# Optimization experiments

Hardware: AMD Instinct MI355X
Metric: run time of the kernel (lower is better)

The kernel has to match this reference:

```python
import jax, jax.numpy as jnp
import numpy as np

B, N = 2, 512
CS, CZ = 512, 128
H, C, PQ, PV = 8, 16, 8, 12
INF, EPS = 1e5, 1e-8


def _points(s, W, b, P):
    # OpenFold layout: [*, N, 3*H*P] split into 3 chunks (x, y, z), stacked on last dim
    p = (s @ W + b).reshape(s.shape[0], s.shape[1], 3, H, P)
    return jnp.moveaxis(p, 2, -1)  # [b, n, H, P, 3]


def setup_inputs() -> dict:
    key = jax.random.key(0)
    ks = jax.random.split(key, 10)
    sc = 0.02
    cat_dim = H * C + H * PV * 4 + H * CZ  # o, o_pt(x,y,z), o_pt_norm, o_pair
    return {
        "seqs": jax.random.normal(ks[0], (B, N, CS), jnp.float32),
        "pair_rep": jax.random.normal(ks[1], (B, N, N, CZ), jnp.float32) * 0.1,
        "x_t": jax.random.normal(ks[2], (B, N, 3), jnp.float32) * 10.0,
        "mask": jnp.ones((B, N), jnp.float32),
        "Wq": jax.random.normal(ks[3], (CS, H * C), jnp.float32) * sc,
        "bq": jnp.zeros((H * C,), jnp.float32),
        "Wkv": jax.random.normal(ks[4], (CS, H * 2 * C), jnp.float32) * sc,
        "bkv": jnp.zeros((H * 2 * C,), jnp.float32),
        "Wqp": jax.random.normal(ks[5], (CS, H * PQ * 3), jnp.float32) * sc,
        "bqp": jnp.zeros((H * PQ * 3,), jnp.float32),
        "Wkvp": jax.random.normal(ks[6], (CS, H * (PQ + PV) * 3), jnp.float32) * sc,
        "bkvp": jnp.zeros((H * (PQ + PV) * 3,), jnp.float32),
        "Wb": jax.random.normal(ks[7], (CZ, H), jnp.float32) * sc,
        "bb": jnp.zeros((H,), jnp.float32),
        "head_w": jnp.zeros((H,), jnp.float32),
        "Wout": jax.random.normal(ks[8], (cat_dim, CS), jnp.float32) * sc,
        "bout": jnp.zeros((CS,), jnp.float32),
    }


def reference(seqs, pair_rep, x_t, mask, Wq, bq, Wkv, bkv, Wqp, bqp, Wkvp, bkvp,
              Wb, bb, head_w, Wout, bout):
    b, n = seqs.shape[0], seqs.shape[1]
    t = x_t * mask[..., None]  # masked translations; rotations are identity

    # scalar q, k, v
    q = (seqs @ Wq + bq).reshape(b, n, H, C)
    kv = (seqs @ Wkv + bkv).reshape(b, n, H, 2 * C)
    k, v = kv[..., :C], kv[..., C:]

    # point q, k, v in global frame (identity rotation => just translate)
    q_pts = _points(seqs, Wqp, bqp, PQ) + t[:, :, None, None, :]      # [b,n,H,PQ,3]
    kv_pts = _points(seqs, Wkvp, bkvp, PQ + PV) + t[:, :, None, None, :]
    k_pts, v_pts = kv_pts[:, :, :, :PQ], kv_pts[:, :, :, PQ:]          # [b,n,H,PQ|PV,3]

    # pair bias
    bias = pair_rep @ Wb + bb                                          # [b,n,n,H]

    # scalar attention logits
    w_l = np.sqrt(1.0 / (3 * C)).astype(np.float32)
    a = jnp.einsum('bihc,bjhc->bhij', q, k) * w_l
    a = a + np.sqrt(1.0 / 3).astype(np.float32) * jnp.transpose(bias, (0, 3, 1, 2))

    # point attention: sum_p |q_ihp - k_jhp|^2 = |q|^2 + |k|^2 - 2 q.k (summed over p,xyz)
    sq_q = jnp.transpose(jnp.sum(q_pts ** 2, axis=(-1, -2)), (0, 2, 1))  # [b,H,n]
    sq_k = jnp.transpose(jnp.sum(k_pts ** 2, axis=(-1, -2)), (0, 2, 1))
    cross = jnp.einsum('bihpx,bjhpx->bhij', q_pts, k_pts)
    d2 = sq_q[..., :, None] + sq_k[..., None, :] - 2.0 * cross           # [b,H,i,j]
    w_c = np.sqrt(1.0 / (3 * (PQ * 9.0 / 2))).astype(np.float32)
    hw = jax.nn.softplus(head_w) * w_c                                   # [H]
    a = a - 0.5 * hw[None, :, None, None] * d2

    # mask
    sq_mask = INF * (mask[:, :, None] * mask[:, None, :] - 1.0)          # [b,n,n]
    a = jax.nn.softmax(a + sq_mask[:, None], axis=-1)                    # [b,H,i,j]

    # outputs
    o = jnp.einsum('bhij,bjhc->bihc', a, v).reshape(b, n, H * C)
    o_pt = jnp.einsum('bhij,bjhpx->bihpx', a, v_pts)                     # [b,n,H,PV,3]
    o_pt = o_pt - t[:, :, None, None, :]                                 # invert_apply (identity rot)
    o_pt_norm = jnp.sqrt(jnp.sum(o_pt ** 2, axis=-1) + EPS).reshape(b, n, H * PV)
    o_pt_flat = o_pt.reshape(b, n, H * PV, 3)
    o_pt_xyz = jnp.concatenate([o_pt_flat[..., 0], o_pt_flat[..., 1], o_pt_flat[..., 2]], axis=-1)
    o_pair = jnp.einsum('bhij,bijz->bihz', a, pair_rep).reshape(b, n, H * CZ)

    feats = jnp.concatenate([o, o_pt_xyz, o_pt_norm, o_pair], axis=-1)
    delta = feats @ Wout + bout
    return (seqs + delta) * mask[..., None]
```

## Files before the change

kernel.cpp:

```cpp
#include <hip/hip_runtime.h>
#include <hip/hip_bf16.h>
#include <math.h>

#define NB 2
#define NN 512
#define DCS 512
#define DCZ 128
#define NH 8
#define DC 16
#define NPQ 8
#define NPV 12

static constexpr float W_L  = 0.14433756729740643f;
static constexpr float W_C  = 0.09622504486493764f;
static constexpr float S13  = 0.57735026918962576f;
static constexpr float F_INF = 100000.0f;
static constexpr float F_EPS = 1e-8f;

static constexpr size_t OFF_Q   = 0;
static constexpr size_t OFF_K   = 131072;
static constexpr size_t OFF_VT  = 262144;
static constexpr size_t OFF_QP  = 393216;
static constexpr size_t OFF_KP  = 589824;
static constexpr size_t OFF_VPT = 786432;
static constexpr size_t OFF_FT  = 1081344;

__global__ __launch_bounds__(320) void k_proj(
    const float* __restrict__ seqs, const float* __restrict__ x_t, const float* __restrict__ mask,
    const float* __restrict__ Wq,  const float* __restrict__ bq,
    const float* __restrict__ Wkv, const float* __restrict__ bkv,
    const float* __restrict__ Wqp, const float* __restrict__ bqp,
    const float* __restrict__ Wkvp,const float* __restrict__ bkvp,
    float* __restrict__ ws)
{
  const int r0 = blockIdx.x * 4;
  __shared__ float s[4][DCS];
  __shared__ float t[4][3];
  {
    float4* s4 = (float4*)s;
    const float4* src4 = (const float4*)(seqs + (size_t)r0 * DCS);
    for (int idx = threadIdx.x; idx < 512; idx += 320) s4[idx] = src4[idx];
    if (threadIdx.x < 12) {
      int r = threadIdx.x / 3, x = threadIdx.x % 3;
      t[r][x] = x_t[(r0 + r)*3 + x] * mask[r0 + r];
    }
  }
  __syncthreads();

  const int qd = threadIdx.x;
  if (qd >= 264) return;

  float* q   = ws + OFF_Q;
  float* kk  = ws + OFF_K;
  float* vT  = ws + OFF_VT;
  float* qp  = ws + OFF_QP;
  float* kp  = ws + OFF_KP;
  float* vpT = ws + OFF_VPT;

  const float* W; const float* bias; int c, ncol, kind;
  if (qd < 32)       { W = Wq;   bias = bq;   c = qd*4;       ncol = 128; kind = 0; }
  else if (qd < 96)  { W = Wkv;  bias = bkv;  c = (qd-32)*4;  ncol = 256; kind = 1; }
  else if (qd < 144) { W = Wqp;  bias = bqp;  c = (qd-96)*4;  ncol = 192; kind = 2; }
  else               { W = Wkvp; bias = bkvp; c = (qd-144)*4; ncol = 480; kind = 3; }

  const float4 b4 = *(const float4*)(bias + c);
  float4 a0 = b4, a1 = b4, a2 = b4, a3 = b4;
  const float* Wp = W + c;

  for (int k = 0; k < DCS; k += 4) {
    float4 w0 = *(const float4*)(Wp + (size_t)(k+0)*ncol);
    float4 w1 = *(const float4*)(Wp + (size_t)(k+1)*ncol);
    float4 w2 = *(const float4*)(Wp + (size_t)(k+2)*ncol);
    float4 w3 = *(const float4*)(Wp + (size_t)(k+3)*ncol);
    float4 s0 = *(const float4*)&s[0][k];
    float4 s1 = *(const float4*)&s[1][k];
    float4 s2 = *(const float4*)&s[2][k];
    float4 s3 = *(const float4*)&s[3][k];
    a0.x = fmaf(s0.x,w0.x, fmaf(s0.y,w1.x, fmaf(s0.z,w2.x, fmaf(s0.w,w3.x, a0.x))));
    a0.y = fmaf(s0.x,w0.y, fmaf(s0.y,w1.y, fmaf(s0.z,w2.y, fmaf(s0.w,w3.y, a0.y))));
    a0.z = fmaf(s0.x,w0.z, fmaf(s0.y,w1.z, fmaf(s0.z,w2.z, fmaf(s0.w,w3.z, a0.z))));
    a0.w = fmaf(s0.x,w0.w, fmaf(s0.y,w1.w, fmaf(s0.z,w2.w, fmaf(s0.w,w3.w, a0.w))));
    a1.x = fmaf(s1.x,w0.x, fmaf(s1.y,w1.x, fmaf(s1.z,w2.x, fmaf(s1.w,w3.x, a1.x))));
    a1.y = fmaf(s1.x,w0.y, fmaf(s1.y,w1.y, fmaf(s1.z,w2.y, fmaf(s1.w,w3.y, a1.y))));
    a1.z = fmaf(s1.x,w0.z, fmaf(s1.y,w1.z, fmaf(s1.z,w2.z, fmaf(s1.w,w3.z, a1.z))));
    a1.w = fmaf(s1.x,w0.w, fmaf(s1.y,w1.w, fmaf(s1.z,w2.w, fmaf(s1.w,w3.w, a1.w))));
    a2.x = fmaf(s2.x,w0.x, fmaf(s2.y,w1.x, fmaf(s2.z,w2.x, fmaf(s2.w,w3.x, a2.x))));
    a2.y = fmaf(s2.x,w0.y, fmaf(s2.y,w1.y, fmaf(s2.z,w2.y, fmaf(s2.w,w3.y, a2.y))));
    a2.z = fmaf(s2.x,w0.z, fmaf(s2.y,w1.z, fmaf(s2.z,w2.z, fmaf(s2.w,w3.z, a2.z))));
    a2.w = fmaf(s2.x,w0.w, fmaf(s2.y,w1.w, fmaf(s2.z,w2.w, fmaf(s2.w,w3.w, a2.w))));
    a3.x = fmaf(s3.x,w0.x, fmaf(s3.y,w1.x, fmaf(s3.z,w2.x, fmaf(s3.w,w3.x, a3.x))));
    a3.y = fmaf(s3.x,w0.y, fmaf(s3.y,w1.y, fmaf(s3.z,w2.y, fmaf(s3.w,w3.y, a3.y))));
    a3.z = fmaf(s3.x,w0.z, fmaf(s3.y,w1.z, fmaf(s3.z,w2.z, fmaf(s3.w,w3.z, a3.z))));
    a3.w = fmaf(s3.x,w0.w, fmaf(s3.y,w1.w, fmaf(s3.z,w2.w, fmaf(s3.w,w3.w, a3.w))));
  }

  float4 accs[4] = {a0, a1, a2, a3};
  #pragma unroll
  for (int r = 0; r < 4; ++r) {
    const int row = r0 + r;
    const int bb_ = row >> 9, j = row & 511;
    float4 acc = accs[r];
    float vals[4] = {acc.x, acc.y, acc.z, acc.w};
    if (kind == 0) {
      *(float4*)(q + (size_t)row*128 + c) = acc;
    } else if (kind == 1) {
      int h = c >> 5, rr = c & 31;
      if (rr < 16) {
        *(float4*)(kk + (size_t)row*128 + h*16 + rr) = acc;
      } else {
        int cp = h*16 + (rr - 16);
        #pragma unroll
        for (int u = 0; u < 4; ++u)
          vT[((size_t)bb_*128 + cp + u)*512 + j] = vals[u];
      }
    } else if (kind == 2) {
      #pragma unroll
      for (int u = 0; u < 4; ++u) {
        int cc = c + u, x = cc >> 6, rem = cc & 63, h = rem >> 3, p = rem & 7;
        qp[(size_t)row*192 + (h*8+p)*3 + x] = vals[u] + t[r][x];
      }
    } else {
      #pragma unroll
      for (int u = 0; u < 4; ++u) {
        int cc = c + u, x = cc / 160, rem = cc % 160, h = rem / 20, p = rem % 20;
        float vv = vals[u] + t[r][x];
        if (p < 8) kp[(size_t)row*192 + (h*8+p)*3 + x] = vv;
        else       vpT[((size_t)bb_*288 + (h*36 + (p-8)*3 + x))*512 + j] = vv;
      }
    }
  }
}

__global__ __launch_bounds__(512) void k_attn(
    const float* __restrict__ pair, const float* __restrict__ x_t, const float* __restrict__ mask,
    const float* __restrict__ head_w, const float* __restrict__ Wb, const float* __restrict__ bb,
    float* __restrict__ ws)
{
  const int row = blockIdx.x;
  const int b = row >> 9, i = row & 511;
  const int tid = threadIdx.x;

  const float* q   = ws + OFF_Q;
  const float* kk  = ws + OFF_K;
  const float* vT  = ws + OFF_VT;
  const float* qp  = ws + OFF_QP;
  const float* kp  = ws + OFF_KP;
  const float* vpT = ws + OFF_VPT;
  float* feats = ws + OFF_FT;

  __shared__ float sA[NH][NN];
  __shared__ float sWb[NH * DCZ];
  __shared__ float sOP[NH * DCZ];
  __shared__ float sQ[128];
  __shared__ float sQP[192];
  __shared__ float sOPT[288];
  __shared__ float sHW[NH];
  __shared__ float sT[3];
  __shared__ float sMi;

  for (int idx = tid; idx < NH*DCZ; idx += 512) {
    int h = idx >> 7, z = idx & 127;
    sWb[idx] = Wb[z*NH + h];
    sOP[idx] = 0.f;
  }
  if (tid < 128) sQ[tid] = q[(size_t)row*128 + tid];
  else if (tid < 320) sQP[tid-128] = qp[(size_t)row*192 + (tid-128)];
  else if (tid < 328) {
    float x = head_w[tid-320];
    float sp = (x > 20.f) ? x : log1pf(expf(x));
    sHW[tid-320] = 0.5f * W_C * sp;
  }
  else if (tid == 328) sMi = mask[row];
  else if (tid >= 336 && tid < 339) sT[tid-336] = x_t[row*3 + (tid-336)] * mask[row];
  __syncthreads();

  {
    const int j = tid;
    const float mj = mask[b*NN + j];
    const float mterm = F_INF * (sMi * mj - 1.0f);

    float accb[NH];
    #pragma unroll
    for (int h = 0; h < NH; ++h) accb[h] = bb[h];
    const float4* prow4 = (const float4*)(pair + ((size_t)(b*NN + i)*NN + j) * DCZ);
    const float4* sWb4  = (const float4*)sWb;
    #pragma unroll 4
    for (int zc = 0; zc < 32; ++zc) {
      float4 pv = prow4[zc];
      #pragma unroll
      for (int h = 0; h < NH; ++h) {
        float4 w = sWb4[h*32 + zc];
        accb[h] = fmaf(pv.x, w.x, fmaf(pv.y, w.y, fmaf(pv.z, w.z, fmaf(pv.w, w.w, accb[h]))));
      }
    }

    const float* kr  = kk + (size_t)(b*NN + j) * 128;
    const float* kpr = kp + (size_t)(b*NN + j) * 192;
    #pragma unroll
    for (int h = 0; h < NH; ++h) {
      float dot = 0.f;
      const float4* k4 = (const float4*)(kr + h*16);
      const float4* q4 = (const float4*)(sQ + h*16);
      #pragma unroll
      for (int u = 0; u < 4; ++u) {
        float4 a = q4[u], cc = k4[u];
        dot += a.x*cc.x + a.y*cc.y + a.z*cc.z + a.w*cc.w;
      }
      float d2 = 0.f;
      const float4* qp4 = (const float4*)(sQP + h*24);
      const float4* kp4 = (const float4*)(kpr + h*24);
      #pragma unroll
      for (int u = 0; u < 6; ++u) {
        float4 a = qp4[u], cc = kp4[u];
        float dx = a.x-cc.x, dy = a.y-cc.y, dz = a.z-cc.z, dw = a.w-cc.w;
        d2 += dx*dx + dy*dy + dz*dz + dw*dw;
      }
      sA[h][j] = W_L * dot + S13 * accb[h] - sHW[h]*d2 + mterm;
    }
  }
  __syncthreads();

  {
    const int h = tid >> 6, lane = tid & 63;
    float vals[8]; float m = -3.0e38f;
    #pragma unroll
    for (int r = 0; r < 8; ++r) { vals[r] = sA[h][lane + 64*r]; m = fmaxf(m, vals[r]); }
    #pragma unroll
    for (int off = 32; off; off >>= 1) m = fmaxf(m, __shfl_xor(m, off, 64));
    float ssum = 0.f;
    #pragma unroll
    for (int r = 0; r < 8; ++r) { vals[r] = __expf(vals[r] - m); ssum += vals[r]; }
    #pragma unroll
    for (int off = 32; off; off >>= 1) ssum += __shfl_xor(ssum, off, 64);
    const float inv = 1.0f / ssum;
    #pragma unroll
    for (int r = 0; r < 8; ++r) sA[h][lane + 64*r] = vals[r] * inv;
  }
  __syncthreads();

  if (tid < 128) {
    const int h = tid >> 4;
    const float4* vr = (const float4*)(vT + ((size_t)b*128 + tid)*512);
    float acc = 0.f;
    #pragma unroll 4
    for (int jg = 0; jg < 128; ++jg) {
      float4 pv = vr[jg];
      float4 av = *(const float4*)&sA[h][jg*4];
      acc = fmaf(pv.x, av.x, fmaf(pv.y, av.y, fmaf(pv.z, av.z, fmaf(pv.w, av.w, acc))));
    }
    feats[(size_t)row*1536 + tid] = acc;
  } else if (tid < 416) {
    const int idx = tid - 128;
    const int h = idx / 36, r2 = idx % 36, x = r2 % 3;
    const float4* vr = (const float4*)(vpT + ((size_t)b*288 + idx)*512);
    float acc = 0.f;
    #pragma unroll 4
    for (int jg = 0; jg < 128; ++jg) {
      float4 pv = vr[jg];
      float4 av = *(const float4*)&sA[h][jg*4];
      acc = fmaf(pv.x, av.x, fmaf(pv.y, av.y, fmaf(pv.z, av.z, fmaf(pv.w, av.w, acc))));
    }
    acc -= sT[x];
    sOPT[idx] = acc;
    feats[(size_t)row*1536 + 128 + x*96 + h*12 + (r2/3)] = acc;
  }
  __syncthreads();

  if (tid < 96) {
    float xx = sOPT[tid*3], yy = sOPT[tid*3+1], zz = sOPT[tid*3+2];
    feats[(size_t)row*1536 + 416 + tid] = sqrtf(xx*xx + yy*yy + zz*zz + F_EPS);
  }

  {
    const int w = tid >> 6, l = tid & 63;
    const int jh = l >> 5, z4 = l & 31;
    const float4* pr4 = (const float4*)(pair + ((size_t)(b*NN + i)) * NN * DCZ);
    float4 acc[NH];
    #pragma unroll
    for (int h = 0; h < NH; ++h) acc[h] = make_float4(0.f,0.f,0.f,0.f);
    const int jbase = w*64;
    #pragma unroll 2
    for (int it = 0; it < 32; ++it) {
      const int j = jbase + it*2 + jh;
      float4 p = pr4[(size_t)j*32 + z4];
      #pragma unroll
      for (int h = 0; h < NH; ++h) {
        float a = sA[h][j];
        acc[h].x = fmaf(a, p.x, acc[h].x);
        acc[h].y = fmaf(a, p.y, acc[h].y);
        acc[h].z = fmaf(a, p.z, acc[h].z);
        acc[h].w = fmaf(a, p.w, acc[h].w);
      }
    }
    #pragma unroll
    for (int h = 0; h < NH; ++h) {
      acc[h].x += __shfl_xor(acc[h].x, 32);
      acc[h].y += __shfl_xor(acc[h].y, 32);
      acc[h].z += __shfl_xor(acc[h].z, 32);
      acc[h].w += __shfl_xor(acc[h].w, 32);
    }
    if (jh == 0) {
      #pragma unroll
      for (int h = 0; h < NH; ++h) {
        float* dst = &sOP[h*DCZ + z4*4];
        atomicAdd(dst+0, acc[h].x);
        atomicAdd(dst+1, acc[h].y);
        atomicAdd(dst+2, acc[h].z);
        atomicAdd(dst+3, acc[h].w);
      }
    }
  }
  __syncthreads();
  for (int idx = tid; idx < NH*DCZ; idx += 512)
    feats[(size_t)row*1536 + 512 + idx] = sOP[idx];
}

__global__ __launch_bounds__(512) void k_out(
    const float* __restrict__ Wout, const float* __restrict__ bout,
    const float* __restrict__ seqs, const float* __restrict__ mask,
    const float* __restrict__ ws, float* __restrict__ out)
{
  const int r0 = blockIdx.x * 8;
  const int tid = threadIdx.x;
  const float* feats = ws + OFF_FT;

  __shared__ float s[8][1536];
  {
    float4* s4 = (float4*)s;
    const float4* f4 = (const float4*)(feats + (size_t)r0*1536);
    for (int idx = tid; idx < 3072; idx += 512) s4[idx] = f4[idx];
  }
  __syncthreads();

  const int qd = tid & 127, kh = tid >> 7;
  const int c = qd*4;
  float4 acc[8];
  #pragma unroll
  for (int r = 0; r < 8; ++r) acc[r] = make_float4(0.f,0.f,0.f,0.f);

  const int kb = kh*384;
  const float* Wp = Wout + c;
  for (int k = kb; k < kb + 384; k += 4) {
    float4 w0 = *(const float4*)(Wp + (size_t)(k+0)*512);
    float4 w1 = *(const float4*)(Wp + (size_t)(k+1)*512);
    float4 w2 = *(const float4*)(Wp + (size_t)(k+2)*512);
    float4 w3 = *(const float4*)(Wp + (size_t)(k+3)*512);
    #pragma unroll
    for (int r = 0; r < 8; ++r) {
      float4 sv = *(const float4*)&s[r][k];
      acc[r].x = fmaf(sv.x,w0.x, fmaf(sv.y,w1.x, fmaf(sv.z,w2.x, fmaf(sv.w,w3.x, acc[r].x))));
      acc[r].y = fmaf(sv.x,w0.y, fmaf(sv.y,w1.y, fmaf(sv.z,w2.y, fmaf(sv.w,w3.y, acc[r].y))));
      acc[r].z = fmaf(sv.x,w0.z, fmaf(sv.y,w1.z, fmaf(sv.z,w2.z, fmaf(sv.w,w3.z, acc[r].z))));
      acc[r].w = fmaf(sv.x,w0.w, fmaf(sv.y,w1.w, fmaf(sv.z,w2.w, fmaf(sv.w,w3.w, acc[r].w))));
    }
  }
  __syncthreads();

  float* part = &s[0][0];
  if (kh > 0) {
    #pragma unroll
    for (int r = 0; r < 8; ++r)
      *(float4*)&part[(((kh-1)*8 + r)*128 + qd)*4] = acc[r];
  }
  __syncthreads();
  if (kh == 0) {
    #pragma unroll
    for (int g = 0; g < 3; ++g) {
      #pragma unroll
      for (int r = 0; r < 8; ++r) {
        float4 p = *(const float4*)&part[((g*8 + r)*128 + qd)*4];
        acc[r].x += p.x; acc[r].y += p.y; acc[r].z += p.z; acc[r].w += p.w;
      }
    }
    float4 bv = *(const float4*)(bout + c);
    #pragma unroll
    for (int r = 0; r < 8; ++r) {
      const int row = r0 + r;
      const float m = mask[row];
      float4 sq = *(const float4*)(seqs + (size_t)row*512 + c);
      float4 o;
      o.x = (sq.x + bv.x + acc[r].x) * m;
      o.y = (sq.y + bv.y + acc[r].y) * m;
      o.z = (sq.z + bv.z + acc[r].z) * m;
      o.w = (sq.w + bv.w + acc[r].w) * m;
      *(float4*)(out + (size_t)row*512 + c) = o;
    }
  }
}

extern "C" void kernel_launch(void* const* d_in, const int* in_sizes, int n_in,
                              void* d_out, int out_size, void* d_ws, size_t ws_size,
                              hipStream_t stream)
{
  const float* seqs   = (const float*)d_in[0];
  const float* pair   = (const float*)d_in[1];
  const float* x_t    = (const float*)d_in[2];
  const float* mask   = (const float*)d_in[3];
  const float* Wq     = (const float*)d_in[4];
  const float* bq     = (const float*)d_in[5];
  const float* Wkv    = (const float*)d_in[6];
  const float* bkv    = (const float*)d_in[7];
  const float* Wqp    = (const float*)d_in[8];
  const float* bqp    = (const float*)d_in[9];
  const float* Wkvp   = (const float*)d_in[10];
  const float* bkvp   = (const float*)d_in[11];
  const float* Wb     = (const float*)d_in[12];
  const float* bb     = (const float*)d_in[13];
  const float* head_w = (const float*)d_in[14];
  const float* Wout   = (const float*)d_in[15];
  const float* bout   = (const float*)d_in[16];
  float* out = (float*)d_out;
  float* ws  = (float*)d_ws;

  hipLaunchKernelGGL(k_proj, dim3(NB*NN/4), dim3(320), 0, stream,
                     seqs, x_t, mask, Wq, bq, Wkv, bkv, Wqp, bqp, Wkvp, bkvp, ws);
  hipLaunchKernelGGL(k_attn, dim3(NB*NN), dim3(512), 0, stream,
                     pair, x_t, mask, head_w, Wb, bb, ws);
  hipLaunchKernelGGL(k_out, dim3(NB*NN/8), dim3(512), 0, stream,
                     Wout, bout, seqs, mask, ws, out);
}
```

Before: 820.1 us.

## Process two query rows per attention block and split-K the projection kernels

k_attn now handles two query rows per block, so each key/value/point load from global memory and each Wb shared read serves both rows. The pair-rep weighted sum is also reorganised so each half-wave covers one row. k_proj moves to 2 rows per block with a two-way K split reduced through shared memory, and k_out to 4 rows per block, both to raise the number of blocks and improve parallelism. The cost is more registers and shared memory per attention block, which may reduce occupancy.

```diff
diff --git a/kernel.cpp b/kernel.cpp
--- a/kernel.cpp
+++ b/kernel.cpp
@@ -25,7 +25,7 @@
 static constexpr size_t OFF_VPT = 786432;
 static constexpr size_t OFF_FT  = 1081344;
 
-__global__ __launch_bounds__(320) void k_proj(
+__global__ __launch_bounds__(528) void k_proj(
     const float* __restrict__ seqs, const float* __restrict__ x_t, const float* __restrict__ mask,
     const float* __restrict__ Wq,  const float* __restrict__ bq,
     const float* __restrict__ Wkv, const float* __restrict__ bkv,
@@ -33,22 +33,24 @@
     const float* __restrict__ Wkvp,const float* __restrict__ bkvp,
     float* __restrict__ ws)
 {
-  const int r0 = blockIdx.x * 4;
-  __shared__ float s[4][DCS];
-  __shared__ float t[4][3];
+  const int r0 = blockIdx.x * 2;
+  const int tid = threadIdx.x;
+  __shared__ float s[2][DCS];
+  __shared__ float t[2][3];
+  __shared__ float pb[2][4][264];
   {
     float4* s4 = (float4*)s;
     const float4* src4 = (const float4*)(seqs + (size_t)r0 * DCS);
-    for (int idx = threadIdx.x; idx < 512; idx += 320) s4[idx] = src4[idx];
-    if (threadIdx.x < 12) {
-      int r = threadIdx.x / 3, x = threadIdx.x % 3;
+    for (int idx = tid; idx < 256; idx += 528) s4[idx] = src4[idx];
+    if (tid < 6) {
+      int r = tid / 3, x = tid % 3;
       t[r][x] = x_t[(r0 + r)*3 + x] * mask[r0 + r];
     }
   }
   __syncthreads();
 
-  const int qd = threadIdx.x;
-  if (qd >= 264) return;
+  const int kh = (tid >= 264) ? 1 : 0;
+  const int qd = tid - kh*264;
 
   float* q   = ws + OFF_Q;
   float* kk  = ws + OFF_K;
@@ -63,19 +65,19 @@
   else if (qd < 144) { W = Wqp;  bias = bqp;  c = (qd-96)*4;  ncol = 192; kind = 2; }
   else               { W = Wkvp; bias = bkvp; c = (qd-144)*4; ncol = 480; kind = 3; }
 
-  const float4 b4 = *(const float4*)(bias + c);
-  float4 a0 = b4, a1 = b4, a2 = b4, a3 = b4;
+  float4 a0, a1;
+  if (kh == 0) { a0 = *(const float4*)(bias + c); a1 = a0; }
+  else         { a0 = make_float4(0.f,0.f,0.f,0.f); a1 = a0; }
   const float* Wp = W + c;
-
-  for (int k = 0; k < DCS; k += 4) {
+  const int kb = kh * 256;
+
+  for (int k = kb; k < kb + 256; k += 4) {
     float4 w0 = *(const float4*)(Wp + (size_t)(k+0)*ncol);
     float4 w1 = *(const float4*)(Wp + (size_t)(k+1)*ncol);
     float4 w2 = *(const float4*)(Wp + (size_t)(k+2)*ncol);
     float4 w3 = *(const float4*)(Wp + (size_t)(k+3)*ncol);
     float4 s0 = *(const float4*)&s[0][k];
     float4 s1 = *(const float4*)&s[1][k];
-    float4 s2 = *(const float4*)&s[2][k];
-    float4 s3 = *(const float4*)&s[3][k];
     a0.x = fmaf(s0.x,w0.x, fmaf(s0.y,w1.x, fmaf(s0.z,w2.x, fmaf(s0.w,w3.x, a0.x))));
     a0.y = fmaf(s0.x,w0.y, fmaf(s0.y,w1.y, fmaf(s0.z,w2.y, fmaf(s0.w,w3.y, a0.y))));
     a0.z = fmaf(s0.x,w0.z, fmaf(s0.y,w1.z, fmaf(s0.z,w2.z, fmaf(s0.w,w3.z, a0.z))));
@@ -84,48 +86,49 @@
     a1.y = fmaf(s1.x,w0.y, fmaf(s1.y,w1.y, fmaf(s1.z,w2.y, fmaf(s1.w,w3.y, a1.y))));
     a1.z = fmaf(s1.x,w0.z, fmaf(s1.y,w1.z, fmaf(s1.z,w2.z, fmaf(s1.w,w3.z, a1.z))));
     a1.w = fmaf(s1.x,w0.w, fmaf(s1.y,w1.w, fmaf(s1.z,w2.w, fmaf(s1.w,w3.w, a1.w))));
-    a2.x = fmaf(s2.x,w0.x, fmaf(s2.y,w1.x, fmaf(s2.z,w2.x, fmaf(s2.w,w3.x, a2.x))));
-    a2.y = fmaf(s2.x,w0.y, fmaf(s2.y,w1.y, fmaf(s2.z,w2.y, fmaf(s2.w,w3.y, a2.y))));
-    a2.z = fmaf(s2.x,w0.z, fmaf(s2.y,w1.z, fmaf(s2.z,w2.z, fmaf(s2.w,w3.z, a2.z))));
-    a2.w = fmaf(s2.x,w0.w, fmaf(s2.y,w1.w, fmaf(s2.z,w2.w, fmaf(s2.w,w3.w, a2.w))));
-    a3.x = fmaf(s3.x,w0.x, fmaf(s3.y,w1.x, fmaf(s3.z,w2.x, fmaf(s3.w,w3.x, a3.x))));
-    a3.y = fmaf(s3.x,w0.y, fmaf(s3.y,w1.y, fmaf(s3.z,w2.y, fmaf(s3.w,w3.y, a3.y))));
-    a3.z = fmaf(s3.x,w0.z, fmaf(s3.y,w1.z, fmaf(s3.z,w2.z, fmaf(s3.w,w3.z, a3.z))));
-    a3.w = fmaf(s3.x,w0.w, fmaf(s3.y,w1.w, fmaf(s3.z,w2.w, fmaf(s3.w,w3.w, a3.w))));
-  }
-
-  float4 accs[4] = {a0, a1, a2, a3};
-  #pragma unroll
-  for (int r = 0; r < 4; ++r) {
-    const int row = r0 + r;
-    const int bb_ = row >> 9, j = row & 511;
-    float4 acc = accs[r];
-    float vals[4] = {acc.x, acc.y, acc.z, acc.w};
-    if (kind == 0) {
-      *(float4*)(q + (size_t)row*128 + c) = acc;
-    } else if (kind == 1) {
-      int h = c >> 5, rr = c & 31;
-      if (rr < 16) {
-        *(float4*)(kk + (size_t)row*128 + h*16 + rr) = acc;
+  }
+
+  if (kh == 1) {
+    pb[0][0][qd] = a0.x; pb[0][1][qd] = a0.y; pb[0][2][qd] = a0.z; pb[0][3][qd] = a0.w;
+    pb[1][0][qd] = a1.x; pb[1][1][qd] = a1.y; pb[1][2][qd] = a1.z; pb[1][3][qd] = a1.w;
+  }
+  __syncthreads();
+  if (kh == 0) {
+    a0.x += pb[0][0][qd]; a0.y += pb[0][1][qd]; a0.z += pb[0][2][qd]; a0.w += pb[0][3][qd];
+    a1.x += pb[1][0][qd]; a1.y += pb[1][1][qd]; a1.z += pb[1][2][qd]; a1.w += pb[1][3][qd];
+    float4 accs[2] = {a0, a1};
+    #pragma unroll
+    for (int r = 0; r < 2; ++r) {
+      const int row = r0 + r;
+      const int bb_ = row >> 9, j = row & 511;
+      float4 acc = accs[r];
+      float vals[4] = {acc.x, acc.y, acc.z, acc.w};
+      if (kind == 0) {
+        *(float4*)(q + (size_t)row*128 + c) = acc;
+      } else if (kind == 1) {
+        int h = c >> 5, rr = c & 31;
+        if (rr < 16) {
+          *(float4*)(kk + (size_t)row*128 + h*16 + rr) = acc;
+        } else {
+          int cp = h*16 + (rr - 16);
+          #pragma unroll
+          for (int u = 0; u < 4; ++u)
+            vT[((size_t)bb_*128 + cp + u)*512 + j] = vals[u];
+        }
+      } else if (kind == 2) {
+        #pragma unroll
+        for (int u = 0; u < 4; ++u) {
+          int cc = c + u, x = cc >> 6, rem = cc & 63, h = rem >> 3, p = rem & 7;
+          qp[(size_t)row*192 + (h*8+p)*3 + x] = vals[u] + t[r][x];
+        }
       } else {
-        int cp = h*16 + (rr - 16);
         #pragma unroll
-        for (int u = 0; u < 4; ++u)
-          vT[((size_t)bb_*128 + cp + u)*512 + j] = vals[u];
-      }
-    } else if (kind == 2) {
-      #pragma unroll
-      for (int u = 0; u < 4; ++u) {
-        int cc = c + u, x = cc >> 6, rem = cc & 63, h = rem >> 3, p = rem & 7;
-        qp[(size_t)row*192 + (h*8+p)*3 + x] = vals[u] + t[r][x];
-      }
-    } else {
-      #pragma unroll
-      for (int u = 0; u < 4; ++u) {
-        int cc = c + u, x = cc / 160, rem = cc % 160, h = rem / 20, p = rem % 20;
-        float vv = vals[u] + t[r][x];
-        if (p < 8) kp[(size_t)row*192 + (h*8+p)*3 + x] = vv;
-        else       vpT[((size_t)bb_*288 + (h*36 + (p-8)*3 + x))*512 + j] = vv;
+        for (int u = 0; u < 4; ++u) {
+          int cc = c + u, x = cc / 160, rem = cc % 160, h = rem / 20, p = rem % 20;
+          float vv = vals[u] + t[r][x];
+          if (p < 8) kp[(size_t)row*192 + (h*8+p)*3 + x] = vv;
+          else       vpT[((size_t)bb_*288 + (h*36 + (p-8)*3 + x))*512 + j] = vv;
+        }
       }
     }
   }
@@ -136,8 +139,10 @@
     const float* __restrict__ head_w, const float* __restrict__ Wb, const float* __restrict__ bb,
     float* __restrict__ ws)
 {
-  const int row = blockIdx.x;
-  const int b = row >> 9, i = row & 511;
+  const int gid = blockIdx.x;
+  const int b = gid >> 8;
+  const int ii = (gid & 255) * 2;
+  const int row0 = b*NN + ii;
   const int tid = threadIdx.x;
 
   const float* q   = ws + OFF_Q;
@@ -148,49 +153,63 @@
   const float* vpT = ws + OFF_VPT;
   float* feats = ws + OFF_FT;
 
-  __shared__ float sA[NH][NN];
+  __shared__ float sA[2][NH][NN];
   __shared__ float sWb[NH * DCZ];
-  __shared__ float sOP[NH * DCZ];
-  __shared__ float sQ[128];
-  __shared__ float sQP[192];
-  __shared__ float sOPT[288];
+  __shared__ float sOP[2][NH * DCZ];
+  __shared__ float sQ[2][128];
+  __shared__ float sQP[2][192];
+  __shared__ float sOPT[2][288];
   __shared__ float sHW[NH];
-  __shared__ float sT[3];
-  __shared__ float sMi;
+  __shared__ float sT[2][3];
+  __shared__ float sMi[2];
 
   for (int idx = tid; idx < NH*DCZ; idx += 512) {
     int h = idx >> 7, z = idx & 127;
     sWb[idx] = Wb[z*NH + h];
-    sOP[idx] = 0.f;
-  }
-  if (tid < 128) sQ[tid] = q[(size_t)row*128 + tid];
-  else if (tid < 320) sQP[tid-128] = qp[(size_t)row*192 + (tid-128)];
-  else if (tid < 328) {
-    float x = head_w[tid-320];
+  }
+  {
+    float* sOPf = &sOP[0][0];
+    for (int idx = tid; idx < 2*NH*DCZ; idx += 512) sOPf[idx] = 0.f;
+  }
+  for (int idx = tid; idx < 640; idx += 512) {
+    if (idx < 256) sQ[idx>>7][idx&127] = q[(size_t)(row0 + (idx>>7))*128 + (idx&127)];
+    else {
+      int k2 = idx - 256; int r = k2/192, cc = k2%192;
+      sQP[r][cc] = qp[(size_t)(row0+r)*192 + cc];
+    }
+  }
+  if (tid < NH) {
+    float x = head_w[tid];
     float sp = (x > 20.f) ? x : log1pf(expf(x));
-    sHW[tid-320] = 0.5f * W_C * sp;
-  }
-  else if (tid == 328) sMi = mask[row];
-  else if (tid >= 336 && tid < 339) sT[tid-336] = x_t[row*3 + (tid-336)] * mask[row];
+    sHW[tid] = 0.5f * W_C * sp;
+  } else if (tid >= 64 && tid < 66) {
+    sMi[tid-64] = mask[row0 + (tid-64)];
+  } else if (tid >= 128 && tid < 134) {
+    int k2 = tid - 128; int r = k2/3, x = k2%3;
+    sT[r][x] = x_t[(row0+r)*3 + x] * mask[row0+r];
+  }
   __syncthreads();
 
   {
     const int j = tid;
     const float mj = mask[b*NN + j];
-    const float mterm = F_INF * (sMi * mj - 1.0f);
-
-    float accb[NH];
-    #pragma unroll
-    for (int h = 0; h < NH; ++h) accb[h] = bb[h];
-    const float4* prow4 = (const float4*)(pair + ((size_t)(b*NN + i)*NN + j) * DCZ);
-    const float4* sWb4  = (const float4*)sWb;
-    #pragma unroll 4
+    const float mterm0 = F_INF * (sMi[0]*mj - 1.0f);
+    const float mterm1 = F_INF * (sMi[1]*mj - 1.0f);
+
+    float accb0[NH], accb1[NH];
+    #pragma unroll
+    for (int h = 0; h < NH; ++h) { accb0[h] = bb[h]; accb1[h] = bb[h]; }
+    const float4* pr0 = (const float4*)(pair + ((size_t)(row0+0)*NN + j) * DCZ);
+    const float4* pr1 = (const float4*)(pair + ((size_t)(row0+1)*NN + j) * DCZ);
+    const float4* sWb4 = (const float4*)sWb;
+    #pragma unroll 2
     for (int zc = 0; zc < 32; ++zc) {
-      float4 pv = prow4[zc];
+      float4 p0 = pr0[zc], p1 = pr1[zc];
       #pragma unroll
       for (int h = 0; h < NH; ++h) {
         float4 w = sWb4[h*32 + zc];
-        accb[h] = fmaf(pv.x, w.x, fmaf(pv.y, w.y, fmaf(pv.z, w.z, fmaf(pv.w, w.w, accb[h]))));
+        accb0[h] = fmaf(p0.x, w.x, fmaf(p0.y, w.y, fmaf(p0.z, w.z, fmaf(p0.w, w.w, accb0[h]))));
+        accb1[h] = fmaf(p1.x, w.x, fmaf(p1.y, w.y, fmaf(p1.z, w.z, fmaf(p1.w, w.w, accb1[h]))));
       }
     }
 
@@ -198,94 +217,110 @@
     const float* kpr = kp + (size_t)(b*NN + j) * 192;
     #pragma unroll
     for (int h = 0; h < NH; ++h) {
-      float dot = 0.f;
-      const float4* k4 = (const float4*)(kr + h*16);
-      const float4* q4 = (const float4*)(sQ + h*16);
+      const float4* k4  = (const float4*)(kr + h*16);
+      const float4* q04 = (const float4*)(&sQ[0][h*16]);
+      const float4* q14 = (const float4*)(&sQ[1][h*16]);
+      float dot0 = 0.f, dot1 = 0.f;
       #pragma unroll
       for (int u = 0; u < 4; ++u) {
-        float4 a = q4[u], cc = k4[u];
-        dot += a.x*cc.x + a.y*cc.y + a.z*cc.z + a.w*cc.w;
-      }
-      float d2 = 0.f;
-      const float4* qp4 = (const float4*)(sQP + h*24);
-      const float4* kp4 = (const float4*)(kpr + h*24);
+        float4 kv = k4[u], a0 = q04[u], a1 = q14[u];
+        dot0 += a0.x*kv.x + a0.y*kv.y + a0.z*kv.z + a0.w*kv.w;
+        dot1 += a1.x*kv.x + a1.y*kv.y + a1.z*kv.z + a1.w*kv.w;
+      }
+      const float4* kp4  = (const float4*)(kpr + h*24);
+      const float4* qp04 = (const float4*)(&sQP[0][h*24]);
+      const float4* qp14 = (const float4*)(&sQP[1][h*24]);
+      float d20 = 0.f, d21 = 0.f;
       #pragma unroll
       for (int u = 0; u < 6; ++u) {
-        float4 a = qp4[u], cc = kp4[u];
-        float dx = a.x-cc.x, dy = a.y-cc.y, dz = a.z-cc.z, dw = a.w-cc.w;
-        d2 += dx*dx + dy*dy + dz*dz + dw*dw;
-      }
-      sA[h][j] = W_L * dot + S13 * accb[h] - sHW[h]*d2 + mterm;
-    }
-  }
-  __syncthreads();
-
-  {
-    const int h = tid >> 6, lane = tid & 63;
-    float vals[8]; float m = -3.0e38f;
-    #pragma unroll
-    for (int r = 0; r < 8; ++r) { vals[r] = sA[h][lane + 64*r]; m = fmaxf(m, vals[r]); }
-    #pragma unroll
-    for (int off = 32; off; off >>= 1) m = fmaxf(m, __shfl_xor(m, off, 64));
-    float ssum = 0.f;
-    #pragma unroll
-    for (int r = 0; r < 8; ++r) { vals[r] = __expf(vals[r] - m); ssum += vals[r]; }
-    #pragma unroll
-    for (int off = 32; off; off >>= 1) ssum += __shfl_xor(ssum, off, 64);
-    const float inv = 1.0f / ssum;
-    #pragma unroll
-    for (int r = 0; r < 8; ++r) sA[h][lane + 64*r] = vals[r] * inv;
+        float4 kv = kp4[u], a0 = qp04[u], a1 = qp14[u];
+        float dx0 = a0.x-kv.x, dy0 = a0.y-kv.y, dz0 = a0.z-kv.z, dw0 = a0.w-kv.w;
+        float dx1 = a1.x-kv.x, dy1 = a1.y-kv.y, dz1 = a1.z-kv.z, dw1 = a1.w-kv.w;
+        d20 += dx0*dx0 + dy0*dy0 + dz0*dz0 + dw0*dw0;
+        d21 += dx1*dx1 + dy1*dy1 + dz1*dz1 + dw1*dw1;
+      }
+      sA[0][h][j] = W_L * dot0 + S13 * accb0[h] - sHW[h]*d20 + mterm0;
+      sA[1][h][j] = W_L * dot1 + S13 * accb1[h] - sHW[h]*d21 + mterm1;
+    }
+  }
+  __syncthreads();
+
+  {
+    const int w = tid >> 6, lane = tid & 63;
+    #pragma unroll
+    for (int r = 0; r < 2; ++r) {
+      float vals[8]; float m = -3.0e38f;
+      #pragma unroll
+      for (int u = 0; u < 8; ++u) { vals[u] = sA[r][w][lane + 64*u]; m = fmaxf(m, vals[u]); }
+      #pragma unroll
+      for (int off = 32; off; off >>= 1) m = fmaxf(m, __shfl_xor(m, off, 64));
+      float ssum = 0.f;
+      #pragma unroll
+      for (int u = 0; u < 8; ++u) { vals[u] = __expf(vals[u] - m); ssum += vals[u]; }
+      #pragma unroll
+      for (int off = 32; off; off >>= 1) ssum += __shfl_xor(ssum, off, 64);
+      const float inv = 1.0f / ssum;
+      #pragma unroll
+      for (int u = 0; u < 8; ++u) sA[r][w][lane + 64*u] = vals[u] * inv;
+    }
   }
   __syncthreads();
 
   if (tid < 128) {
-    const int h = tid >> 4;
-    const float4* vr = (const float4*)(vT + ((size_t)b*128 + tid)*512);
-    float acc = 0.f;
+    const int cc = tid, h = tid >> 4;
+    const float4* vr = (const float4*)(vT + ((size_t)b*128 + cc)*512);
+    float acc0 = 0.f, acc1 = 0.f;
     #pragma unroll 4
     for (int jg = 0; jg < 128; ++jg) {
       float4 pv = vr[jg];
-      float4 av = *(const float4*)&sA[h][jg*4];
-      acc = fmaf(pv.x, av.x, fmaf(pv.y, av.y, fmaf(pv.z, av.z, fmaf(pv.w, av.w, acc))));
-    }
-    feats[(size_t)row*1536 + tid] = acc;
+      float4 a0 = *(const float4*)&sA[0][h][jg*4];
+      float4 a1 = *(const float4*)&sA[1][h][jg*4];
+      acc0 = fmaf(pv.x, a0.x, fmaf(pv.y, a0.y, fmaf(pv.z, a0.z, fmaf(pv.w, a0.w, acc0))));
+      acc1 = fmaf(pv.x, a1.x, fmaf(pv.y, a1.y, fmaf(pv.z, a1.z, fmaf(pv.w, a1.w, acc1))));
+    }
+    feats[(size_t)(row0+0)*1536 + cc] = acc0;
+    feats[(size_t)(row0+1)*1536 + cc] = acc1;
   } else if (tid < 416) {
     const int idx = tid - 128;
     const int h = idx / 36, r2 = idx % 36, x = r2 % 3;
     const float4* vr = (const float4*)(vpT + ((size_t)b*288 + idx)*512);
-    float acc = 0.f;
+    float acc0 = 0.f, acc1 = 0.f;
     #pragma unroll 4
     for (int jg = 0; jg < 128; ++jg) {
       float4 pv = vr[jg];
-      float4 av = *(const float4*)&sA[h][jg*4];
-      acc = fmaf(pv.x, av.x, fmaf(pv.y, av.y, fmaf(pv.z, av.z, fmaf(pv.w, av.w, acc))));
-    }
-    acc -= sT[x];
-    sOPT[idx] = acc;
-    feats[(size_t)row*1536 + 128 + x*96 + h*12 + (r2/3)] = acc;
-  }
-  __syncthreads();
-
-  if (tid < 96) {
-    float xx = sOPT[tid*3], yy = sOPT[tid*3+1], zz = sOPT[tid*3+2];
-    feats[(size_t)row*1536 + 416 + tid] = sqrtf(xx*xx + yy*yy + zz*zz + F_EPS);
+      float4 a0 = *(const float4*)&sA[0][h][jg*4];
+      float4 a1 = *(const float4*)&sA[1][h][jg*4];
+      acc0 = fmaf(pv.x, a0.x, fmaf(pv.y, a0.y, fmaf(pv.z, a0.z, fmaf(pv.w, a0.w, acc0))));
+      acc1 = fmaf(pv.x, a1.x, fmaf(pv.y, a1.y, fmaf(pv.z, a1.z, fmaf(pv.w, a1.w, acc1))));
+    }
+    acc0 -= sT[0][x]; acc1 -= sT[1][x];
+    sOPT[0][idx] = acc0; sOPT[1][idx] = acc1;
+    feats[(size_t)(row0+0)*1536 + 128 + x*96 + h*12 + (r2/3)] = acc0;
+    feats[(size_t)(row0+1)*1536 + 128 + x*96 + h*12 + (r2/3)] = acc1;
+  }
+  __syncthreads();
+
+  if (tid < 192) {
+    int r = tid / 96, p = tid % 96;
+    float xx = sOPT[r][p*3], yy = sOPT[r][p*3+1], zz = sOPT[r][p*3+2];
+    feats[(size_t)(row0+r)*1536 + 416 + p] = sqrtf(xx*xx + yy*yy + zz*zz + F_EPS);
   }
 
   {
     const int w = tid >> 6, l = tid & 63;
-    const int jh = l >> 5, z4 = l & 31;
-    const float4* pr4 = (const float4*)(pair + ((size_t)(b*NN + i)) * NN * DCZ);
+    const int r = l >> 5, z4 = l & 31;
+    const int jbase = w * 64;
+    const float4* prp = (const float4*)(pair + (size_t)(row0 + r) * NN * DCZ);
     float4 acc[NH];
     #pragma unroll
     for (int h = 0; h < NH; ++h) acc[h] = make_float4(0.f,0.f,0.f,0.f);
-    const int jbase = w*64;
     #pragma unroll 2
-    for (int it = 0; it < 32; ++it) {
-      const int j = jbase + it*2 + jh;
-      float4 p = pr4[(size_t)j*32 + z4];
+    for (int it = 0; it < 64; ++it) {
+      const int j = jbase + it;
+      float4 p = prp[(size_t)j*32 + z4];
       #pragma unroll
       for (int h = 0; h < NH; ++h) {
-        float a = sA[h][j];
+        float a = sA[r][h][j];
         acc[h].x = fmaf(a, p.x, acc[h].x);
         acc[h].y = fmaf(a, p.y, acc[h].y);
         acc[h].z = fmaf(a, p.z, acc[h].z);
@@ -294,25 +329,21 @@
     }
     #pragma unroll
     for (int h = 0; h < NH; ++h) {
-      acc[h].x += __shfl_xor(acc[h].x, 32);
-      acc[h].y += __shfl_xor(acc[h].y, 32);
-      acc[h].z += __shfl_xor(acc[h].z, 32);
-      acc[h].w += __shfl_xor(acc[h].w, 32);
-    }
-    if (jh == 0) {
-      #pragma unroll
-      for (int h = 0; h < NH; ++h) {
-        float* dst = &sOP[h*DCZ + z4*4];
-        atomicAdd(dst+0, acc[h].x);
-        atomicAdd(dst+1, acc[h].y);
-        atomicAdd(dst+2, acc[h].z);
-        atomicAdd(dst+3, acc[h].w);
-      }
-    }
-  }
-  __syncthreads();
-  for (int idx = tid; idx < NH*DCZ; idx += 512)
-    feats[(size_t)row*1536 + 512 + idx] = sOP[idx];
+      float* dst = &sOP[r][h*DCZ + z4*4];
+      atomicAdd(dst+0, acc[h].x);
+      atomicAdd(dst+1, acc[h].y);
+      atomicAdd(dst+2, acc[h].z);
+      atomicAdd(dst+3, acc[h].w);
+    }
+  }
+  __syncthreads();
+  {
+    const float* sOPf = &sOP[0][0];
+    for (int idx = tid; idx < 2048; idx += 512) {
+      int r = idx >> 10, z = idx & 1023;
+      feats[(size_t)(row0+r)*1536 + 512 + z] = sOPf[idx];
+    }
+  }
 }
 
 __global__ __launch_bounds__(512) void k_out(
@@ -320,23 +351,24 @@
     const float* __restrict__ seqs, const float* __restrict__ mask,
     const float* __restrict__ ws, float* __restrict__ out)
 {
-  const int r0 = blockIdx.x * 8;
+  const int r0 = blockIdx.x * 4;
   const int tid = threadIdx.x;
   const float* feats = ws + OFF_FT;
 
-  __shared__ float s[8][1536];
+  __shared__ float s[4][1536];
+  __shared__ float pb[3][4][4][128];
   {
     float4* s4 = (float4*)s;
     const float4* f4 = (const float4*)(feats + (size_t)r0*1536);
-    for (int idx = tid; idx < 3072; idx += 512) s4[idx] = f4[idx];
+    for (int idx = tid; idx < 1536; idx += 512) s4[idx] = f4[idx];
   }
   __syncthreads();
 
   const int qd = tid & 127, kh = tid >> 7;
   const int c = qd*4;
-  float4 acc[8];
+  float4 acc[4];
   #pragma unroll
-  for (int r = 0; r < 8; ++r) acc[r] = make_float4(0.f,0.f,0.f,0.f);
+  for (int r = 0; r < 4; ++r) acc[r] = make_float4(0.f,0.f,0.f,0.f);
 
   const int kb = kh*384;
   const float* Wp = Wout + c;
@@ -346,7 +378,7 @@
     float4 w2 = *(const float4*)(Wp + (size_t)(k+2)*512);
     float4 w3 = *(const float4*)(Wp + (size_t)(k+3)*512);
     #pragma unroll
-    for (int r = 0; r < 8; ++r) {
+    for (int r = 0; r < 4; ++r) {
       float4 sv = *(const float4*)&s[r][k];
       acc[r].x = fmaf(sv.x,w0.x, fmaf(sv.y,w1.x, fmaf(sv.z,w2.x, fmaf(sv.w,w3.x, acc[r].x))));
       acc[r].y = fmaf(sv.x,w0.y, fmaf(sv.y,w1.y, fmaf(sv.z,w2.y, fmaf(sv.w,w3.y, acc[r].y))));
@@ -354,27 +386,31 @@
       acc[r].w = fmaf(sv.x,w0.w, fmaf(sv.y,w1.w, fmaf(sv.z,w2.w, fmaf(sv.w,w3.w, acc[r].w))));
     }
   }
-  __syncthreads();
-
-  float* part = &s[0][0];
+
   if (kh > 0) {
     #pragma unroll
-    for (int r = 0; r < 8; ++r)
-      *(float4*)&part[(((kh-1)*8 + r)*128 + qd)*4] = acc[r];
+    for (int r = 0; r < 4; ++r) {
+      pb[kh-1][r][0][qd] = acc[r].x;
+      pb[kh-1][r][1][qd] = acc[r].y;
+      pb[kh-1][r][2][qd] = acc[r].z;
+      pb[kh-1][r][3][qd] = acc[r].w;
+    }
   }
   __syncthreads();
   if (kh == 0) {
     #pragma unroll
     for (int g = 0; g < 3; ++g) {
       #pragma unroll
-      for (int r = 0; r < 8; ++r) {
-        float4 p = *(const float4*)&part[((g*8 + r)*128 + qd)*4];
-        acc[r].x += p.x; acc[r].y += p.y; acc[r].z += p.z; acc[r].w += p.w;
+      for (int r = 0; r < 4; ++r) {
+        acc[r].x += pb[g][r][0][qd];
+        acc[r].y += pb[g][r][1][qd];
+        acc[r].z += pb[g][r][2][qd];
+        acc[r].w += pb[g][r][3][qd];
       }
     }
     float4 bv = *(const float4*)(bout + c);
     #pragma unroll
-    for (int r = 0; r < 8; ++r) {
+    for (int r = 0; r < 4; ++r) {
       const int row = r0 + r;
       const float m = mask[row];
       float4 sq = *(const float4*)(seqs + (size_t)row*512 + c);
@@ -412,10 +448,10 @@
   float* out = (float*)d_out;
   float* ws  = (float*)d_ws;
 
-  hipLaunchKernelGGL(k_proj, dim3(NB*NN/4), dim3(320), 0, stream,
+  hipLaunchKernelGGL(k_proj, dim3(NB*NN/2), dim3(528), 0, stream,
                      seqs, x_t, mask, Wq, bq, Wkv, bkv, Wqp, bqp, Wkvp, bkvp, ws);
-  hipLaunchKernelGGL(k_attn, dim3(NB*NN), dim3(512), 0, stream,
+  hipLaunchKernelGGL(k_attn, dim3(NB*NN/2), dim3(512), 0, stream,
                      pair, x_t, mask, head_w, Wb, bb, ws);
-  hipLaunchKernelGGL(k_out, dim3(NB*NN/8), dim3(512), 0, stream,
+  hipLaunchKernelGGL(k_out, dim3(NB*NN/4), dim3(512), 0, stream,
                      Wout, bout, seqs, mask, ws, out);
 }
```

After: 730.3 us. 10.9% less time.
